# Kernel optimization log

Measured on AMD Instinct MI355X. Metric: run time of the kernel, lower is better.

Reference implementation:

```python
import jax, jax.numpy as jnp
import numpy as np

N_TOKENS = 1024
HIDDEN = 2048
N_EXPERTS = 16
MOE_INTER = 1024
TOP_K = 6
N_GROUP = 4
TOPK_GROUP = 2
N_SHARED = 2
ROUTED_SCALING = 2.5
RENORM = True
CAPACITY = 1024  # >> N_TOKENS*TOP_K/N_EXPERTS = 384; overflow probability negligible


def setup_inputs() -> dict:
    key = jax.random.key(0)
    ks = jax.random.split(key, 7)
    s = 0.02
    return {
        'hidden_states': jax.random.normal(ks[0], (N_TOKENS, HIDDEN), jnp.float32),
        'gate_w': jax.random.normal(ks[1], (N_EXPERTS, HIDDEN), jnp.float32) * s,
        'gate_bias': jax.random.normal(ks[2], (N_EXPERTS,), jnp.float32) * s,
        'w_gate_up': jax.random.normal(ks[3], (N_EXPERTS, HIDDEN, 2 * MOE_INTER), jnp.float32) * s,
        'w_down': jax.random.normal(ks[4], (N_EXPERTS, MOE_INTER, HIDDEN), jnp.float32) * s,
        'shared_w_gate_up': jax.random.normal(ks[5], (HIDDEN, 2 * N_SHARED * MOE_INTER), jnp.float32) * s,
        'shared_w_down': jax.random.normal(ks[6], (N_SHARED * MOE_INTER, HIDDEN), jnp.float32) * s,
    }


def _swiglu(gu):
    # npu_swiglu with activate_left=True: silu(first half) * second half
    g, u = jnp.split(gu, 2, axis=-1)
    return jax.nn.silu(g) * u


def reference(hidden_states, gate_w, gate_bias, w_gate_up, w_down, shared_w_gate_up, shared_w_down):
    x = hidden_states
    N, H = x.shape
    E, K, C = N_EXPERTS, TOP_K, CAPACITY
    P = N * K  # number of (token, slot) pairs

    # ---- MoEGate: router logits + noaux_tc grouped top-k ----
    logits = x @ gate_w.T                              # [N, E]
    scores = jax.nn.sigmoid(logits)                    # sigmoid scoring (noaux_tc)
    s_corr = scores + gate_bias[None, :]
    sg = s_corr.reshape(N, N_GROUP, E // N_GROUP)
    group_scores = jax.lax.top_k(sg, 2)[0].sum(-1)     # top-2 sum per group [N, G]
    _, gidx = jax.lax.top_k(group_scores, TOPK_GROUP)
    gmask = jnp.sum(jax.nn.one_hot(gidx, N_GROUP, dtype=jnp.float32), axis=1) > 0
    masked = jnp.where(gmask[:, :, None], sg, -jnp.inf).reshape(N, E)
    _, topk_ids = jax.lax.top_k(masked, K)             # [N, K]
    w = jnp.take_along_axis(scores, topk_ids, axis=-1)  # weights from original scores
    if RENORM:
        w = w / jnp.sum(w, axis=-1, keepdims=True)
    w = w * ROUTED_SCALING

    # ---- dispatch: fixed-capacity buffers per expert ----
    flat_e = topk_ids.reshape(P)
    onehot = jax.nn.one_hot(flat_e, E, dtype=jnp.int32)
    pos = jnp.cumsum(onehot, axis=0)[jnp.arange(P), flat_e] - 1  # slot within expert
    valid = pos < C
    buf = jnp.full((E, C), P, jnp.int32).at[flat_e, jnp.clip(pos, 0, C - 1)].set(
        jnp.where(valid, jnp.arange(P, dtype=jnp.int32), P))
    tok = jnp.where(buf < P, buf // K, N)              # token index per slot, N = pad
    x_pad = jnp.concatenate([x, jnp.zeros((1, H), x.dtype)], axis=0)
    xe = x_pad[tok]                                    # [E, C, H]

    # ---- grouped expert GEMMs (SwiGLU MLP per expert) ----
    h = jnp.einsum('ech,ehi->eci', xe, w_gate_up)      # [E, C, 2I]
    y = jnp.einsum('eci,eih->ech', _swiglu(h), w_down)  # [E, C, H]

    # ---- combine: weighted scatter-add back to tokens ----
    w_pad = jnp.concatenate([w.reshape(P), jnp.zeros((1,), w.dtype)])
    pw = w_pad[jnp.where(buf < P, buf, P)]             # [E, C]
    routed = jnp.zeros((N + 1, H), x.dtype).at[tok].add(y * pw[:, :, None])[:N]

    # ---- shared experts (reduce_results=False, fused add) ----
    shared = _swiglu(x @ shared_w_gate_up) @ shared_w_down
    return routed + shared
```

## Files before the change

### kernel.cpp

```cpp
#include <hip/hip_runtime.h>
#include <hip/hip_bf16.h>
#include <math.h>

typedef __attribute__((ext_vector_type(8))) short bf16x8;
typedef __attribute__((ext_vector_type(4))) float f32x4;

#define N_TOK 1024
#define HID   2048
#define NEXP  16
#define NE2   18
#define INTER 1024
#define TOPK  6
#define CAP   1024

__device__ __forceinline__ unsigned short f2bf(float f) {
  unsigned u = __builtin_bit_cast(unsigned, f);
  u += 0x7fffu + ((u >> 16) & 1u);
  return (unsigned short)(u >> 16);
}
__device__ __forceinline__ float b2f(short s) {
  unsigned u = ((unsigned)(unsigned short)s) << 16;
  return __builtin_bit_cast(float, u);
}
__device__ __forceinline__ void gll16(const void* g, void* l) {
  __builtin_amdgcn_global_load_lds(
      (const __attribute__((address_space(1))) unsigned int*)g,
      (__attribute__((address_space(3))) unsigned int*)l, 16, 0, 0);
}
__device__ __forceinline__ void xcd_remap(int& bx, int& by, int& bz) {
  int gx = gridDim.x, gy = gridDim.y;
  int nwg = gx * gy * (int)gridDim.z;
  int lid = bx + gx * (by + gy * bz);
  int q = nwg >> 3, r = nwg & 7;
  int xcd = lid & 7, i = lid >> 3;
  int swz = (xcd < r ? xcd * (q + 1) : r * (q + 1) + (xcd - r) * q) + i;
  bx = swz % gx; int t2 = swz / gx; by = t2 % gy; bz = t2 / gy;
}

__global__ __launch_bounds__(256) void router_k(
    const float* __restrict__ x, const float* __restrict__ gw,
    const float* __restrict__ gb, int* __restrict__ counts,
    int* __restrict__ tok_list, int* __restrict__ meta,
    float* __restrict__ pwt, unsigned short* __restrict__ x_bf)
{
  const int t   = blockIdx.x;
  const int tid = threadIdx.x;
  __shared__ float xrow[HID];
  __shared__ float logits[NEXP];

  for (int i = tid; i < HID; i += 256) {
    float v = x[(size_t)t * HID + i];
    xrow[i] = v;
    x_bf[(size_t)t * HID + i] = f2bf(v);
  }
  __syncthreads();

  const int w = tid >> 6, lane = tid & 63;
  for (int s = 0; s < 4; ++s) {
    int e = w * 4 + s;
    const float* g = gw + (size_t)e * HID;
    float p = 0.f;
    for (int i = lane; i < HID; i += 64) p += xrow[i] * g[i];
    for (int off = 32; off; off >>= 1) p += __shfl_down(p, off);
    if (lane == 0) logits[e] = p;
  }
  __syncthreads();

  if (tid == 0) {
    float sc[NEXP], scorr[NEXP];
    for (int e = 0; e < NEXP; ++e) {
      float s1 = 1.f / (1.f + expf(-logits[e]));
      sc[e] = s1; scorr[e] = s1 + gb[e];
    }
    float gs[4];
    for (int g = 0; g < 4; ++g) {
      float m1 = -1e30f, m2 = -1e30f;
      for (int j = 0; j < 4; ++j) {
        float v = scorr[g * 4 + j];
        if (v > m1) { m2 = m1; m1 = v; } else if (v > m2) m2 = v;
      }
      gs[g] = m1 + m2;
    }
    int g1 = 0;
    for (int g = 1; g < 4; ++g) if (gs[g] > gs[g1]) g1 = g;
    int g2 = -1;
    for (int g = 0; g < 4; ++g) { if (g == g1) continue; if (g2 < 0 || gs[g] > gs[g2]) g2 = g; }

    bool taken[NEXP];
    for (int e = 0; e < NEXP; ++e) taken[e] = false;
    int ids[TOPK]; float wv[TOPK]; float wsum = 0.f;
    for (int k = 0; k < TOPK; ++k) {
      int best = -1; float bv = -1e30f;
      for (int e = 0; e < NEXP; ++e) {
        int grp = e >> 2;
        if (grp != g1 && grp != g2) continue;
        if (taken[e]) continue;
        if (scorr[e] > bv) { bv = scorr[e]; best = e; }
      }
      taken[best] = true; ids[k] = best; wv[k] = sc[best]; wsum += sc[best];
    }
    float inv = 2.5f / wsum;
    for (int k = 0; k < TOPK; ++k) {
      int e = ids[k];
      int slot = atomicAdd(&counts[e], 1);
      tok_list[e * CAP + slot] = t;
      meta[t * TOPK + k] = (e << 16) | slot;
      pwt[t * TOPK + k] = wv[k] * inv;
    }
  }
}

template<int MODE>
__global__ __launch_bounds__(256, 3) void gemm_fw_k(
    const unsigned short* __restrict__ A, int lda, size_t a_estride,
    const float* __restrict__ Wr, const float* __restrict__ Ws, int K,
    const int* __restrict__ counts, const int* __restrict__ tok_list,
    unsigned short* __restrict__ outb, int out_ld, size_t out_estride)
{
  int bx = blockIdx.x, by = blockIdx.y, bz = blockIdx.z;
  xcd_remap(bx, by, bz);
  const int e  = bz;
  const int m0 = by * 128;
  const int M  = (e < 16) ? counts[e] : N_TOK;
  if (m0 >= M) return;
  const int n0 = bx * (MODE == 0 ? 64 : 128);

  __shared__ __align__(16) unsigned short Al[128 * 64];
  __shared__ __align__(16) unsigned short Bl[128 * 64];

  const int tid = threadIdx.x, lane = tid & 63, wid = tid >> 6;
  const int wm = wid >> 1, wn = wid & 1, l15 = lane & 15, hi = lane >> 4;

  const unsigned short* Ap = A + (size_t)e * a_estride;

  const unsigned short* asrc[4]; void* adst[4];
  #pragma unroll
  for (int i = 0; i < 4; ++i) {
    int c = tid + 256 * i;
    int r = c >> 3, s = c & 7, sl = s ^ (r & 7);
    int slot = m0 + r;
    int row;
    if (MODE == 0) row = (e < 16) ? ((slot < M) ? tok_list[e * CAP + slot] : 0) : slot;
    else           row = slot;
    asrc[i] = Ap + (size_t)row * lda + sl * 8;
    adst[i] = (char*)Al + c * 16;
  }

  const int nq = tid & 31, kb8 = tid >> 5;
  const float* bp; int ldw;
  {
    int n_ = nq * 4;
    if (MODE == 0) {
      if (e < 16) {
        size_t col = (n_ < 64) ? (size_t)(n0 + n_) : (size_t)(1024 + n0 + n_ - 64);
        bp = Wr + (size_t)e * HID * (2 * INTER) + col; ldw = 2 * INTER;
      } else {
        int j = e - 16;
        size_t col = (n_ < 64) ? (size_t)(j * 1024 + n0 + n_)
                               : (size_t)(2048 + j * 1024 + n0 + n_ - 64);
        bp = Ws + col; ldw = 4096;
      }
    } else {
      bp = ((e < 16) ? Wr + (size_t)e * INTER * HID
                     : Ws + (size_t)(e - 16) * INTER * HID) + (n0 + n_);
      ldw = HID;
    }
    bp += (size_t)(kb8 * 8) * ldw;
  }
  int bwoff[4];
  {
    int sp = (kb8 ^ (nq & 7)) << 4;
    #pragma unroll
    for (int j = 0; j < 4; ++j) bwoff[j] = (nq * 4 + j) * 128 + sp;
  }

  int bn[4];
  if (MODE == 0) { bn[0] = wn*32; bn[1] = wn*32+16; bn[2] = 64+wn*32; bn[3] = 80+wn*32; }
  else           { bn[0] = wn*64; bn[1] = wn*64+16; bn[2] = wn*64+32; bn[3] = wn*64+48; }

  f32x4 acc[4][4];
  #pragma unroll
  for (int a0 = 0; a0 < 4; ++a0)
    #pragma unroll
    for (int b0 = 0; b0 < 4; ++b0) acc[a0][b0] = (f32x4){0.f, 0.f, 0.f, 0.f};

  for (int kt = 0; kt < K; kt += 64) {
    float4 bf4[8];
    #pragma unroll
    for (int i = 0; i < 8; ++i)
      bf4[i] = *(const float4*)(bp + (size_t)(kt + i) * ldw);
    #pragma unroll
    for (int i = 0; i < 4; ++i) gll16(asrc[i] + kt, adst[i]);
    #pragma unroll
    for (int j = 0; j < 4; ++j) {
      unsigned w4[4];
      #pragma unroll
      for (int p = 0; p < 4; ++p) {
        float lo  = ((const float*)(bf4 + 2 * p))[j];
        float hi2 = ((const float*)(bf4 + 2 * p + 1))[j];
        unsigned rr;
        asm("v_cvt_pk_bf16_f32 %0, %1, %2" : "=v"(rr) : "v"(lo), "v"(hi2));
        w4[p] = rr;
      }
      *(uint4*)((char*)Bl + bwoff[j]) = *(uint4*)w4;
    }
    __syncthreads();

    #pragma unroll
    for (int kk = 0; kk < 64; kk += 32) {
      bf16x8 af[4], bv[4];
      #pragma unroll
      for (int mi = 0; mi < 4; ++mi) {
        int r = wm * 64 + mi * 16 + l15;
        int off = (r * 128 + (kk + hi * 8) * 2) ^ ((r & 7) << 4);
        af[mi] = *(const bf16x8*)((const char*)Al + off);
      }
      #pragma unroll
      for (int ni = 0; ni < 4; ++ni) {
        int r = bn[ni] + l15;
        int off = r * 128 + (((((kk >> 3) + hi)) ^ ((r >> 2) & 7)) << 4);
        bv[ni] = *(const bf16x8*)((const char*)Bl + off);
      }
      #pragma unroll
      for (int mi = 0; mi < 4; ++mi)
        #pragma unroll
        for (int ni = 0; ni < 4; ++ni)
          acc[mi][ni] = __builtin_amdgcn_mfma_f32_16x16x32_bf16(af[mi], bv[ni], acc[mi][ni], 0, 0, 0);
    }
    __syncthreads();
  }

  const int rbase = hi * 4;
  if (MODE == 0) {
    #pragma unroll
    for (int mi = 0; mi < 4; ++mi)
      #pragma unroll
      for (int rr = 0; rr < 4; ++rr) {
        int slot = m0 + wm * 64 + mi * 16 + rbase + rr;
        if (slot >= M) continue;
        #pragma unroll
        for (int j = 0; j < 2; ++j) {
          float g = acc[mi][j][rr], u = acc[mi][j + 2][rr];
          float sv = g / (1.f + expf(-g)) * u;
          int col = n0 + wn * 32 + j * 16 + l15;
          outb[(size_t)e * out_estride + (size_t)slot * out_ld + col] = f2bf(sv);
        }
      }
  } else {
    #pragma unroll
    for (int mi = 0; mi < 4; ++mi)
      #pragma unroll
      for (int rr = 0; rr < 4; ++rr) {
        int slot = m0 + wm * 64 + mi * 16 + rbase + rr;
        if (slot >= M) continue;
        unsigned short* row = outb + (size_t)e * out_estride + (size_t)slot * out_ld;
        #pragma unroll
        for (int ni = 0; ni < 4; ++ni)
          row[n0 + bn[ni] + l15] = f2bf(acc[mi][ni][rr]);
      }
  }
}

__global__ __launch_bounds__(256) void combine_k(
    const unsigned short* __restrict__ ybuf, const int* __restrict__ meta,
    const float* __restrict__ pwt, float* __restrict__ out)
{
  const int t = blockIdx.x;
  const int c0 = threadIdx.x * 8;
  float acc[8];
  {
    bf16x8 v0 = *(const bf16x8*)(ybuf + ((size_t)16 * CAP + t) * HID + c0);
    bf16x8 v1 = *(const bf16x8*)(ybuf + ((size_t)17 * CAP + t) * HID + c0);
    #pragma unroll
    for (int j = 0; j < 8; ++j) acc[j] = b2f(v0[j]) + b2f(v1[j]);
  }
  #pragma unroll
  for (int k = 0; k < TOPK; ++k) {
    int m = meta[t * TOPK + k];
    float w = pwt[t * TOPK + k];
    int e = m >> 16, s = m & 0xffff;
    bf16x8 v = *(const bf16x8*)(ybuf + ((size_t)e * CAP + s) * HID + c0);
    #pragma unroll
    for (int j = 0; j < 8; ++j) acc[j] += w * b2f(v[j]);
  }
  float4* o = (float4*)(out + (size_t)t * HID + c0);
  o[0] = make_float4(acc[0], acc[1], acc[2], acc[3]);
  o[1] = make_float4(acc[4], acc[5], acc[6], acc[7]);
}

extern "C" void kernel_launch(void* const* d_in, const int* in_sizes, int n_in,
                              void* d_out, int out_size, void* d_ws, size_t ws_size,
                              hipStream_t stream) {
  const float* x   = (const float*)d_in[0];
  const float* gw  = (const float*)d_in[1];
  const float* gb  = (const float*)d_in[2];
  const float* wgu = (const float*)d_in[3];
  const float* wd  = (const float*)d_in[4];
  const float* sgu = (const float*)d_in[5];
  const float* sd  = (const float*)d_in[6];
  float* out = (float*)d_out;

  char* ws = (char*)d_ws;
  int*   counts   = (int*)ws;
  int*   tok_list = (int*)(ws + 256);
  int*   meta     = (int*)(ws + 256 + 65536);
  float* pwt      = (float*)(ws + 256 + 65536 + 24576);
  unsigned short* x_bf = (unsigned short*)(ws + 128 * 1024);
  unsigned short* act  = x_bf + (size_t)N_TOK * HID;
  unsigned short* ybuf = act + (size_t)NE2 * CAP * INTER;
  const size_t need = (size_t)((char*)(ybuf + (size_t)NE2 * CAP * HID) - ws);
  if (ws_size < need) return;

  hipMemsetAsync(counts, 0, 256, stream);
  router_k<<<N_TOK, 256, 0, stream>>>(x, gw, gb, counts, tok_list, meta, pwt, x_bf);

  gemm_fw_k<0><<<dim3(INTER / 64, CAP / 128, NE2), 256, 0, stream>>>(
      x_bf, HID, 0, wgu, sgu, HID, counts, tok_list,
      act, INTER, (size_t)CAP * INTER);
  gemm_fw_k<1><<<dim3(HID / 128, CAP / 128, NE2), 256, 0, stream>>>(
      act, INTER, (size_t)CAP * INTER, wd, sd, INTER, counts, nullptr,
      ybuf, HID, (size_t)CAP * HID);

  combine_k<<<N_TOK, 256, 0, stream>>>(ybuf, meta, pwt, out);
}
```

Baseline: 504.9 us.

## Double-buffer LDS tiles in expert GEMM to overlap loads with MFMA

The GEMM main loop now keeps two LDS buffers for the A and B tiles. The next K-tile's A (direct global-to-LDS) and fp32 B loads are issued before the MFMAs on the current tile, and the B conversion and write happen afterwards, which removes the load-then-compute serialization. It also changes the B-tile LDS swizzle with an extra XOR on row bits to cut bank conflicts. LDS use doubles and launch bounds drop from 3 to 2 blocks per CU, so occupancy and register pressure become the trade-off.

```diff
diff --git a/kernel.cpp b/kernel.cpp
--- a/kernel.cpp
+++ b/kernel.cpp
@@ -111,7 +111,7 @@
 }
 
 template<int MODE>
-__global__ __launch_bounds__(256, 3) void gemm_fw_k(
+__global__ __launch_bounds__(256, 2) void gemm_fw_k(
     const unsigned short* __restrict__ A, int lda, size_t a_estride,
     const float* __restrict__ Wr, const float* __restrict__ Ws, int K,
     const int* __restrict__ counts, const int* __restrict__ tok_list,
@@ -125,15 +125,15 @@
   if (m0 >= M) return;
   const int n0 = bx * (MODE == 0 ? 64 : 128);
 
-  __shared__ __align__(16) unsigned short Al[128 * 64];
-  __shared__ __align__(16) unsigned short Bl[128 * 64];
+  __shared__ __align__(16) unsigned short Al[2][128 * 64];
+  __shared__ __align__(16) unsigned short Bl[2][128 * 64];
 
   const int tid = threadIdx.x, lane = tid & 63, wid = tid >> 6;
   const int wm = wid >> 1, wn = wid & 1, l15 = lane & 15, hi = lane >> 4;
 
   const unsigned short* Ap = A + (size_t)e * a_estride;
 
-  const unsigned short* asrc[4]; void* adst[4];
+  const unsigned short* asrc[4]; int aoff[4];
   #pragma unroll
   for (int i = 0; i < 4; ++i) {
     int c = tid + 256 * i;
@@ -143,7 +143,7 @@
     if (MODE == 0) row = (e < 16) ? ((slot < M) ? tok_list[e * CAP + slot] : 0) : slot;
     else           row = slot;
     asrc[i] = Ap + (size_t)row * lda + sl * 8;
-    adst[i] = (char*)Al + c * 16;
+    aoff[i] = c * 16;
   }
 
   const int nq = tid & 31, kb8 = tid >> 5;
@@ -168,11 +168,9 @@
     bp += (size_t)(kb8 * 8) * ldw;
   }
   int bwoff[4];
-  {
-    int sp = (kb8 ^ (nq & 7)) << 4;
-    #pragma unroll
-    for (int j = 0; j < 4; ++j) bwoff[j] = (nq * 4 + j) * 128 + sp;
-  }
+  #pragma unroll
+  for (int j = 0; j < 4; ++j)
+    bwoff[j] = (nq * 4 + j) * 128 + ((kb8 ^ (nq & 7) ^ (j << 1)) << 4);
 
   int bn[4];
   if (MODE == 0) { bn[0] = wn*32; bn[1] = wn*32+16; bn[2] = 64+wn*32; bn[3] = 80+wn*32; }
@@ -184,28 +182,47 @@
     #pragma unroll
     for (int b0 = 0; b0 < 4; ++b0) acc[a0][b0] = (f32x4){0.f, 0.f, 0.f, 0.f};
 
-  for (int kt = 0; kt < K; kt += 64) {
-    float4 bf4[8];
-    #pragma unroll
-    for (int i = 0; i < 8; ++i)
-      bf4[i] = *(const float4*)(bp + (size_t)(kt + i) * ldw);
-    #pragma unroll
-    for (int i = 0; i < 4; ++i) gll16(asrc[i] + kt, adst[i]);
-    #pragma unroll
-    for (int j = 0; j < 4; ++j) {
-      unsigned w4[4];
-      #pragma unroll
-      for (int p = 0; p < 4; ++p) {
-        float lo  = ((const float*)(bf4 + 2 * p))[j];
-        float hi2 = ((const float*)(bf4 + 2 * p + 1))[j];
-        unsigned rr;
-        asm("v_cvt_pk_bf16_f32 %0, %1, %2" : "=v"(rr) : "v"(lo), "v"(hi2));
-        w4[p] = rr;
-      }
-      *(uint4*)((char*)Bl + bwoff[j]) = *(uint4*)w4;
-    }
-    __syncthreads();
-
+  float4 bf4[8];
+  #define LOADB(kt)                                                         \
+    _Pragma("unroll")                                                       \
+    for (int i = 0; i < 8; ++i)                                             \
+      bf4[i] = *(const float4*)(bp + (size_t)((kt) + i) * ldw);
+  #define WRITEB(Bb)                                                        \
+    _Pragma("unroll")                                                       \
+    for (int j = 0; j < 4; ++j) {                                           \
+      unsigned w4[4];                                                       \
+      _Pragma("unroll")                                                     \
+      for (int q2 = 0; q2 < 4; ++q2) {                                      \
+        float lo  = ((const float*)(bf4 + 2 * q2))[j];                      \
+        float hi2 = ((const float*)(bf4 + 2 * q2 + 1))[j];                  \
+        unsigned rr;                                                        \
+        asm("v_cvt_pk_bf16_f32 %0, %1, %2" : "=v"(rr) : "v"(lo), "v"(hi2)); \
+        w4[q2] = rr;                                                        \
+      }                                                                     \
+      *(uint4*)((char*)(Bb) + bwoff[j]) = *(uint4*)w4;                      \
+    }
+
+  LOADB(0)
+  #pragma unroll
+  for (int i = 0; i < 4; ++i) gll16(asrc[i], (char*)Al[0] + aoff[i]);
+  asm volatile("s_waitcnt vmcnt(0)" ::: "memory");
+  WRITEB(Bl[0])
+  __syncthreads();
+
+  const int nt = K >> 6;
+  int p = 0;
+  for (int t = 0; t < nt; ++t) {
+    const bool pf = (t + 1 < nt);
+    if (pf) {
+      const int kt1 = (t + 1) << 6;
+      #pragma unroll
+      for (int i = 0; i < 4; ++i)
+        gll16(asrc[i] + kt1, (char*)Al[p ^ 1] + aoff[i]);
+      LOADB(kt1)
+    }
+
+    const char* Ab = (const char*)Al[p];
+    const char* Bb = (const char*)Bl[p];
     #pragma unroll
     for (int kk = 0; kk < 64; kk += 32) {
       bf16x8 af[4], bv[4];
@@ -213,13 +230,14 @@
       for (int mi = 0; mi < 4; ++mi) {
         int r = wm * 64 + mi * 16 + l15;
         int off = (r * 128 + (kk + hi * 8) * 2) ^ ((r & 7) << 4);
-        af[mi] = *(const bf16x8*)((const char*)Al + off);
+        af[mi] = *(const bf16x8*)(Ab + off);
       }
       #pragma unroll
       for (int ni = 0; ni < 4; ++ni) {
         int r = bn[ni] + l15;
-        int off = r * 128 + (((((kk >> 3) + hi)) ^ ((r >> 2) & 7)) << 4);
-        bv[ni] = *(const bf16x8*)((const char*)Bl + off);
+        int slot = (kk >> 3) + hi;
+        int off = r * 128 + ((slot ^ ((r >> 2) & 7) ^ ((r & 3) << 1)) << 4);
+        bv[ni] = *(const bf16x8*)(Bb + off);
       }
       #pragma unroll
       for (int mi = 0; mi < 4; ++mi)
@@ -227,8 +245,16 @@
         for (int ni = 0; ni < 4; ++ni)
           acc[mi][ni] = __builtin_amdgcn_mfma_f32_16x16x32_bf16(af[mi], bv[ni], acc[mi][ni], 0, 0, 0);
     }
+
+    if (pf) {
+      asm volatile("s_waitcnt vmcnt(0)" ::: "memory");
+      WRITEB(Bl[p ^ 1])
+    }
     __syncthreads();
-  }
+    p ^= 1;
+  }
+  #undef LOADB
+  #undef WRITEB
 
   const int rbase = hi * 4;
   if (MODE == 0) {
```

Measured after the change: 479.0 us. 1.05x faster.
